# Kernel tuning notes

Hardware: AMD Instinct MI355X
Metric: run time of the kernel (lower is better)

Reference implementation:

```python
import jax, jax.numpy as jnp
import numpy as np

BIT_WEIGHTS = jnp.asarray(1 << np.arange(7, -1, -1), dtype=jnp.uint8)  # big-endian bit order


def _packbits_last(bits):
    """Pack 0/1 uint8 bits along the last axis into uint8 bytes (big bitorder).
    bits: [..., N] uint8 in {0,1}. Returns [..., ceil(N/8)] uint8."""
    n = bits.shape[-1]
    pad = (-n) % 8
    if pad:
        bits = jnp.pad(bits, [(0, 0)] * (bits.ndim - 1) + [(0, pad)])
    bits = bits.reshape(bits.shape[:-1] + ((n + pad) // 8, 8))
    # weighted sum over the 8-bit group; max value 255 fits in uint8
    return jnp.sum(bits * BIT_WEIGHTS, axis=-1, dtype=jnp.uint8)


def setup_inputs() -> dict:
    key = jax.random.key(0)
    kx, _ = jax.random.split(key)
    x = jax.random.normal(kx, (4096, 8192), dtype=jnp.float32)  # normalized FP32 input
    depth = jnp.asarray([-0.67, 0.0, 0.67], dtype=jnp.float32)  # TH_DEPTH3 thresholds
    return {"x": x, "depth": depth}


def reference(x, depth):
    # x: [b, i] float32; depth: [D] thresholds
    # compare -> [b, D, i] bits, then pack along last axis -> [b, D, ceil(i/8)] uint8
    bits = (x[:, None, :] > depth[None, :, None]).astype(jnp.uint8)
    return _packbits_last(bits)
```

## Files before the change

### kernel.cpp

```cpp
#include <hip/hip_runtime.h>


typedef float nfloat4 __attribute__((ext_vector_type(4)));

constexpr int ROWS = 4096;
constexpr int COLS = 8192;
constexpr int BYTES_PER_ROW = COLS / 8;
constexpr int TOTAL = ROWS * BYTES_PER_ROW;
constexpr int BLOCK = 256;
constexpr int ITERS = 8;
constexpr int GRID = TOTAL / (BLOCK * ITERS);

__global__ __launch_bounds__(BLOCK) void binarize_pack_kernel(
    const float* __restrict__ x,
    const float* __restrict__ depth,
    int* __restrict__ out) {
    const int tid0 = blockIdx.x * BLOCK + threadIdx.x;
    const int stride = GRID * BLOCK;

    const float d0 = depth[0];
    const float d1 = depth[1];
    const float d2 = depth[2];

#pragma unroll
    for (int it = 0; it < ITERS; ++it) {
        const int tid = tid0 + it * stride;

        const nfloat4* xv = reinterpret_cast<const nfloat4*>(x) + (size_t)tid * 2;
        const nfloat4 a = __builtin_nontemporal_load(xv);
        const nfloat4 b = __builtin_nontemporal_load(xv + 1);

        const float v[8] = {a.x, a.y, a.z, a.w, b.x, b.y, b.z, b.w};

        unsigned p0 = 0, p1 = 0, p2 = 0;
#pragma unroll
        for (int k = 0; k < 8; ++k) {
            const unsigned w = 1u << (7 - k);
            p0 |= (v[k] > d0) ? w : 0u;
            p1 |= (v[k] > d1) ? w : 0u;
            p2 |= (v[k] > d2) ? w : 0u;
        }

        const int row = tid >> 10;
        const int col = tid & 1023;
        int* o = out + (size_t)row * (3 * BYTES_PER_ROW) + col;
        __builtin_nontemporal_store((int)p0, o + 0 * BYTES_PER_ROW);
        __builtin_nontemporal_store((int)p1, o + 1 * BYTES_PER_ROW);
        __builtin_nontemporal_store((int)p2, o + 2 * BYTES_PER_ROW);
    }
}

extern "C" void kernel_launch(void* const* d_in, const int* in_sizes, int n_in,
                              void* d_out, int out_size, void* d_ws, size_t ws_size,
                              hipStream_t stream) {
    const float* x = (const float*)d_in[0];
    const float* depth = (const float*)d_in[1];
    int* out = (int*)d_out;

    binarize_pack_kernel<<<GRID, BLOCK, 0, stream>>>(x, depth, out);
}
```

Before: 197.2 us.

## Process four output words per thread with 128-bit vector stores

Each thread now loads 32 contiguous floats (8 float4 loads) and emits four packed words per depth plane, written as one 128-bit store per plane. The grid-stride loop over eight iterations is replaced by a single-shot mapping with a larger grid. This widens stores and makes each thread's loads contiguous, but each wavefront's loads now stride 128 bytes per lane, which may hurt coalescing, and register pressure rises.

```diff
diff --git a/kernel.cpp b/kernel.cpp
--- a/kernel.cpp
+++ b/kernel.cpp
@@ -2,52 +2,64 @@
 
 
 typedef float nfloat4 __attribute__((ext_vector_type(4)));
+typedef int   nint4   __attribute__((ext_vector_type(4)));
 
 constexpr int ROWS = 4096;
 constexpr int COLS = 8192;
 constexpr int BYTES_PER_ROW = COLS / 8;
 constexpr int TOTAL = ROWS * BYTES_PER_ROW;
 constexpr int BLOCK = 256;
-constexpr int ITERS = 8;
-constexpr int GRID = TOTAL / (BLOCK * ITERS);
+constexpr int GROUPS = TOTAL / 4;
+constexpr int GRID = GROUPS / BLOCK;
 
 __global__ __launch_bounds__(BLOCK) void binarize_pack_kernel(
     const float* __restrict__ x,
     const float* __restrict__ depth,
     int* __restrict__ out) {
-    const int tid0 = blockIdx.x * BLOCK + threadIdx.x;
-    const int stride = GRID * BLOCK;
+    const int g = blockIdx.x * BLOCK + threadIdx.x;
 
     const float d0 = depth[0];
     const float d1 = depth[1];
     const float d2 = depth[2];
 
+    const nfloat4* xv = reinterpret_cast<const nfloat4*>(x) + (size_t)g * 8;
+    nfloat4 r[8];
 #pragma unroll
-    for (int it = 0; it < ITERS; ++it) {
-        const int tid = tid0 + it * stride;
+    for (int i = 0; i < 8; ++i) r[i] = __builtin_nontemporal_load(xv + i);
 
-        const nfloat4* xv = reinterpret_cast<const nfloat4*>(x) + (size_t)tid * 2;
-        const nfloat4 a = __builtin_nontemporal_load(xv);
-        const nfloat4 b = __builtin_nontemporal_load(xv + 1);
+    float v[32];
+#pragma unroll
+    for (int i = 0; i < 8; ++i) {
+        v[4 * i + 0] = r[i].x;
+        v[4 * i + 1] = r[i].y;
+        v[4 * i + 2] = r[i].z;
+        v[4 * i + 3] = r[i].w;
+    }
 
-        const float v[8] = {a.x, a.y, a.z, a.w, b.x, b.y, b.z, b.w};
-
+    nint4 o0, o1, o2;
+#pragma unroll
+    for (int b = 0; b < 4; ++b) {
         unsigned p0 = 0, p1 = 0, p2 = 0;
 #pragma unroll
         for (int k = 0; k < 8; ++k) {
             const unsigned w = 1u << (7 - k);
-            p0 |= (v[k] > d0) ? w : 0u;
-            p1 |= (v[k] > d1) ? w : 0u;
-            p2 |= (v[k] > d2) ? w : 0u;
+            const float val = v[8 * b + k];
+            p0 |= (val > d0) ? w : 0u;
+            p1 |= (val > d1) ? w : 0u;
+            p2 |= (val > d2) ? w : 0u;
         }
+        o0[b] = (int)p0;
+        o1[b] = (int)p1;
+        o2[b] = (int)p2;
+    }
 
-        const int row = tid >> 10;
-        const int col = tid & 1023;
-        int* o = out + (size_t)row * (3 * BYTES_PER_ROW) + col;
-        __builtin_nontemporal_store((int)p0, o + 0 * BYTES_PER_ROW);
-        __builtin_nontemporal_store((int)p1, o + 1 * BYTES_PER_ROW);
-        __builtin_nontemporal_store((int)p2, o + 2 * BYTES_PER_ROW);
-    }
+    const int byte0 = g * 4;
+    const int row = byte0 >> 10;
+    const int col = byte0 & 1023;
+    int* o = out + (size_t)row * (3 * BYTES_PER_ROW) + col;
+    __builtin_nontemporal_store(o0, reinterpret_cast<nint4*>(o + 0 * BYTES_PER_ROW));
+    __builtin_nontemporal_store(o1, reinterpret_cast<nint4*>(o + 1 * BYTES_PER_ROW));
+    __builtin_nontemporal_store(o2, reinterpret_cast<nint4*>(o + 2 * BYTES_PER_ROW));
 }
 
 extern "C" void kernel_launch(void* const* d_in, const int* in_sizes, int n_in,
```

Measured after the change: 233.4 us. +18.3%, slower.
